# Kernel tuning notes

Measured on AMD Instinct MI355X. Metric: run time of the kernel, lower is better.

The kernel has to match this reference:

```python
import jax, jax.numpy as jnp
import numpy as np

H_Q = 32      # num_attention_heads
H_KV = 8      # num_key_value_heads
D = 128       # head_dim
WIN = 127     # left window size (flash window_size=(127,-1))
BLK = 128


def setup_inputs() -> dict:
    key = jax.random.key(0)
    kq, kk, kv = jax.random.split(key, 3)
    B, S = 2, 4096
    Q = jax.random.normal(kq, (B, S, H_Q * D), dtype=jnp.float32)
    K = jax.random.normal(kk, (B, S, H_KV * D), dtype=jnp.float32)
    V = jax.random.normal(kv, (B, S, H_KV * D), dtype=jnp.float32)
    return {"Q": Q, "K": K, "V": V}


def _banded_mask(nblk):
    # query row r in block n has global index n*BLK + r
    # key col c in window indexes global key (n-1)*BLK + c,  c in [0, 2*BLK)
    r = jnp.arange(BLK)[:, None]
    c = jnp.arange(2 * BLK)[None, :]
    base = (c <= r + BLK) & (c >= r + BLK - WIN)          # [BLK, 2BLK]
    n = jnp.arange(nblk)[:, None, None]
    valid_pad = (n > 0) | (c[None] >= BLK)                # block 0 has zero-padded left keys
    return base[None] & valid_pad                          # [nblk, BLK, 2BLK]


def reference(Q, K, V):
    B, S, _ = Q.shape
    nblk = S // BLK
    g = H_Q // H_KV
    scale = 1.0 / np.sqrt(D)

    # [B, Hkv, g, nblk, BLK, D]
    q = Q.reshape(B, S, H_Q, D).transpose(0, 2, 1, 3).reshape(B, H_KV, g, nblk, BLK, D)
    k = K.reshape(B, S, H_KV, D).transpose(0, 2, 1, 3)   # [B, Hkv, S, D]
    v = V.reshape(B, S, H_KV, D).transpose(0, 2, 1, 3)

    # pad one zero block in front, then build 2-block sliding windows
    pad = jnp.zeros((B, H_KV, BLK, D), dtype=K.dtype)
    kp = jnp.concatenate([pad, k], axis=2).reshape(B, H_KV, nblk + 1, BLK, D)
    vp = jnp.concatenate([pad, v], axis=2).reshape(B, H_KV, nblk + 1, BLK, D)
    kwin = jnp.concatenate([kp[:, :, :-1], kp[:, :, 1:]], axis=3)  # [B,Hkv,nblk,2BLK,D]
    vwin = jnp.concatenate([vp[:, :, :-1], vp[:, :, 1:]], axis=3)

    scores = jnp.einsum('bhgnrd,bhncd->bhgnrc', q, kwin) * scale   # [B,Hkv,g,nblk,BLK,2BLK]
    mask = _banded_mask(nblk)                                      # [nblk,BLK,2BLK]
    scores = jnp.where(mask[None, None, None], scores, jnp.finfo(scores.dtype).min)
    p = jax.nn.softmax(scores, axis=-1)
    out = jnp.einsum('bhgnrc,bhncd->bhgnrd', p, vwin)              # [B,Hkv,g,nblk,BLK,D]
    out = out.reshape(B, H_Q, S, D).transpose(0, 2, 1, 3).reshape(B, S, H_Q * D)
    return out
```

## Files before the change

### kernel.cpp

```cpp
#include <hip/hip_runtime.h>
#include <stdint.h>

#define S_LEN 4096
#define HQ 32
#define HKV 8
#define DD 128
#define QBLK 128
#define KVROW (HKV * DD)

typedef __attribute__((ext_vector_type(8)))  __bf16 bf16x8;
typedef __attribute__((ext_vector_type(2)))  __bf16 bf16x2;
typedef __attribute__((ext_vector_type(4)))  float  f32x4;
typedef __attribute__((ext_vector_type(2)))  unsigned int u32x2;
typedef __attribute__((ext_vector_type(4)))  unsigned int u32x4;

__device__ __forceinline__ unsigned int pk2(float lo, float hi2) {
  bf16x2 t = {(__bf16)lo, (__bf16)hi2};
  return __builtin_bit_cast(unsigned int, t);
}
__device__ __forceinline__ bf16x8 mk8(unsigned int w0, unsigned int w1,
                                      unsigned int w2, unsigned int w3) {
  u32x4 u = {w0, w1, w2, w3};
  return __builtin_bit_cast(bf16x8, u);
}

#define SWZV(d) ((((d) & 7) ^ (((d) >> 4) & 7)) << 3)

__global__ __launch_bounds__(512, 4)
void swa_fwd(const float* __restrict__ Qg, const float* __restrict__ Kg,
             const float* __restrict__ Vg, float* __restrict__ Og) {
  __shared__ __align__(16) unsigned char Kl[40960];
  __shared__ __align__(16) unsigned char Vl[40960];

  const int nwg  = gridDim.x;
  const int bid0 = blockIdx.x;
  const int bid  = (bid0 & 7) * (nwg >> 3) + (bid0 >> 3);

  const int j    = bid & 3;
  const int n    = (bid >> 2) & 31;
  const int hkv  = (bid >> 7) & 7;
  const int b    = bid >> 10;
  const int tid  = threadIdx.x;
  const int lane = tid & 63;
  const int wv   = tid >> 6;
  const int g    = lane >> 4;
  const int l15  = lane & 15;

  const int cc = wv & 1;
  const int h  = hkv * 4 + (wv >> 1);
  const int cg = 2 * j + cc;
  const int qrow = n * QBLK + 32 * j + cc * 16 + l15;

  const float* qp = Qg + (size_t)(b * S_LEN + qrow) * (HQ * DD) + h * DD + g * 8;
  bf16x8 qf[4];
  #pragma unroll
  for (int dc = 0; dc < 4; ++dc) {
    f32x4 a  = *(const f32x4*)(qp + dc * 32);
    f32x4 c4 = *(const f32x4*)(qp + dc * 32 + 4);
    qf[dc] = mk8(pk2(a[0], a[1]), pk2(a[2], a[3]),
                 pk2(c4[0], c4[1]), pk2(c4[2], c4[3]));
  }

  const int kbase = (n - 1) * QBLK + 32 * j;
  #pragma unroll
  for (int i = 0; i < 10; ++i) {
    const int e  = i * 512 + tid;
    const int c  = e >> 5;
    const int dc = e & 31;
    int tk = kbase + c;
    tk = tk > 0 ? tk : 0;
    const size_t base = (size_t)(b * S_LEN + tk) * KVROW + hkv * DD + dc * 4;
    const f32x4 xk = *(const f32x4*)(Kg + base);
    const f32x4 xv = *(const f32x4*)(Vg + base);
    u32x2 kw = { pk2(xk[0], xk[1]), pk2(xk[2], xk[3]) };
    *(u32x2*)(&Kl[c * 256 + ((dc * 8) ^ ((c & 15) << 4))]) = kw;
    #pragma unroll
    for (int j4 = 0; j4 < 4; ++j4) {
      const int d = dc * 4 + j4;
      *(unsigned short*)(&Vl[d * 320 + ((c * 2) ^ SWZV(d))]) =
          __builtin_bit_cast(unsigned short, (__bf16)xv[j4]);
    }
  }
  __syncthreads();

  const float SC = 0.08838834764831845f * 1.44269504088896340f;

  f32x4 o[8];
  #pragma unroll
  for (int dt = 0; dt < 8; ++dt) o[dt] = (f32x4){0.f, 0.f, 0.f, 0.f};
  float ls = 0.f;

  #pragma unroll
  for (int pp = 0; pp < 5; ++pp) {
    const int tt0 = 2 * pp, tt1 = 2 * pp + 1;
    if (n == 0 && cg + tt1 < 8) continue;

    unsigned int w0 = 0, w1 = 0, w2 = 0, w3 = 0;

    if (!(n == 0 && cg + tt0 < 8)) {
      const int c = (cc + tt0) * 16 + l15;
      f32x4 acc = {0.f, 0.f, 0.f, 0.f};
      __builtin_amdgcn_s_setprio(1);
      #pragma unroll
      for (int dc = 0; dc < 4; ++dc) {
        const bf16x8 kf = *(const bf16x8*)(
            &Kl[c * 256 + ((dc * 64 + g * 16) ^ ((c & 15) << 4))]);
        acc = __builtin_amdgcn_mfma_f32_16x16x32_bf16(kf, qf[dc], acc, 0, 0, 0);
      }
      __builtin_amdgcn_s_setprio(0);
      float p[4];
      #pragma unroll
      for (int r = 0; r < 4; ++r) {
        const int g4r = g * 4 + r;
        const float e = __builtin_amdgcn_exp2f(acc[r] * SC);
        bool valid = true;
        if (pp == 0) valid = (g4r > l15);
        if (pp == 4) valid = (g4r <= l15);
        p[r] = valid ? e : 0.f;
        ls += p[r];
      }
      w0 = pk2(p[0], p[1]);
      w1 = pk2(p[2], p[3]);
    }

    if (pp < 4 && !(n == 0 && cg + tt1 < 8)) {
      const int c = (cc + tt1) * 16 + l15;
      f32x4 acc = {0.f, 0.f, 0.f, 0.f};
      __builtin_amdgcn_s_setprio(1);
      #pragma unroll
      for (int dc = 0; dc < 4; ++dc) {
        const bf16x8 kf = *(const bf16x8*)(
            &Kl[c * 256 + ((dc * 64 + g * 16) ^ ((c & 15) << 4))]);
        acc = __builtin_amdgcn_mfma_f32_16x16x32_bf16(kf, qf[dc], acc, 0, 0, 0);
      }
      __builtin_amdgcn_s_setprio(0);
      float p0 = __builtin_amdgcn_exp2f(acc[0] * SC);
      float p1 = __builtin_amdgcn_exp2f(acc[1] * SC);
      float p2 = __builtin_amdgcn_exp2f(acc[2] * SC);
      float p3 = __builtin_amdgcn_exp2f(acc[3] * SC);
      ls += p0 + p1 + p2 + p3;
      w2 = pk2(p0, p1);
      w3 = pk2(p2, p3);
    }

    const bf16x8 pf = mk8(w0, w1, w2, w3);
    const int ck0 = ((cc + tt0) * 16 + g * 4) * 2;
    const int ck1 = (pp < 4) ? ((cc + tt1) * 16 + g * 4) * 2 : ck0;
    __builtin_amdgcn_s_setprio(1);
    #pragma unroll
    for (int dt = 0; dt < 8; ++dt) {
      const int d  = dt * 16 + l15;
      const int rb = d * 320;
      const int sz = SWZV(d);
      const u32x2 a0 = *(const u32x2*)(&Vl[rb + (ck0 ^ sz)]);
      const u32x2 a1 = *(const u32x2*)(&Vl[rb + (ck1 ^ sz)]);
      const bf16x8 vf = mk8(a0[0], a0[1], a1[0], a1[1]);
      o[dt] = __builtin_amdgcn_mfma_f32_16x16x32_bf16(vf, pf, o[dt], 0, 0, 0);
    }
    __builtin_amdgcn_s_setprio(0);
  }

  ls += __shfl_xor(ls, 16);
  ls += __shfl_xor(ls, 32);
  const float inv = 1.0f / ls;

  float* op = Og + (size_t)(b * S_LEN + qrow) * (HQ * DD) + h * DD + g * 4;
  #pragma unroll
  for (int dt = 0; dt < 8; ++dt) {
    f32x4 v = o[dt];
    v[0] *= inv; v[1] *= inv; v[2] *= inv; v[3] *= inv;
    *(f32x4*)(op + dt * 16) = v;
  }
}

extern "C" void kernel_launch(void* const* d_in, const int* in_sizes, int n_in,
                              void* d_out, int out_size, void* d_ws, size_t ws_size,
                              hipStream_t stream) {
  const float* Q = (const float*)d_in[0];
  const float* K = (const float*)d_in[1];
  const float* V = (const float*)d_in[2];
  float* O = (float*)d_out;
  const int B = in_sizes[0] / (S_LEN * HQ * DD);
  const int nblocks = B * HKV * (S_LEN / QBLK) * 4;
  swa_fwd<<<dim3(nblocks), dim3(512), 0, stream>>>(Q, K, V, O);
}
```

Measured before the change: 92.37 us.

## Process all four query sub-blocks per workgroup with a rolling K/V ring buffer

Each workgroup now handles the whole 128-row query block in a loop of four 32-row steps instead of launching one workgroup per step. The 160-key K/V window lives in LDS as a ring: after each step, 32 new key rows are written over the oldest slot, and their global loads are issued before the current compute so the latency is hidden. This removes the redundant re-loading and bf16 conversion of overlapping K/V windows across the four former workgroups. In exchange the grid is 4x smaller (512 workgroups), parallelism drops, and two barriers are added per step.

New measurement: 79.78 us, median of 2. 13.6% less time.

```diff
diff --git a/kernel.cpp b/kernel.cpp
--- a/kernel.cpp
+++ b/kernel.cpp
@@ -36,10 +36,9 @@
   const int bid0 = blockIdx.x;
   const int bid  = (bid0 & 7) * (nwg >> 3) + (bid0 >> 3);
 
-  const int j    = bid & 3;
-  const int n    = (bid >> 2) & 31;
-  const int hkv  = (bid >> 7) & 7;
-  const int b    = bid >> 10;
+  const int n    = bid & 31;
+  const int hkv  = (bid >> 5) & 7;
+  const int b    = bid >> 8;
   const int tid  = threadIdx.x;
   const int lane = tid & 63;
   const int wv   = tid >> 6;
@@ -48,32 +47,22 @@
 
   const int cc = wv & 1;
   const int h  = hkv * 4 + (wv >> 1);
-  const int cg = 2 * j + cc;
-  const int qrow = n * QBLK + 32 * j + cc * 16 + l15;
-
-  const float* qp = Qg + (size_t)(b * S_LEN + qrow) * (HQ * DD) + h * DD + g * 8;
-  bf16x8 qf[4];
-  #pragma unroll
-  for (int dc = 0; dc < 4; ++dc) {
-    f32x4 a  = *(const f32x4*)(qp + dc * 32);
-    f32x4 c4 = *(const f32x4*)(qp + dc * 32 + 4);
-    qf[dc] = mk8(pk2(a[0], a[1]), pk2(a[2], a[3]),
-                 pk2(c4[0], c4[1]), pk2(c4[2], c4[3]));
-  }
-
-  const int kbase = (n - 1) * QBLK + 32 * j;
+
+  const int c0 = tid >> 5;
+  const int dc = tid & 31;
+  const size_t kvoff = hkv * DD + dc * 4;
+  const int kbase0 = (n - 1) * QBLK;
+
   #pragma unroll
   for (int i = 0; i < 10; ++i) {
-    const int e  = i * 512 + tid;
-    const int c  = e >> 5;
-    const int dc = e & 31;
-    int tk = kbase + c;
+    const int c = c0 + i * 16;
+    int tk = kbase0 + c;
     tk = tk > 0 ? tk : 0;
-    const size_t base = (size_t)(b * S_LEN + tk) * KVROW + hkv * DD + dc * 4;
+    const size_t base = (size_t)(b * S_LEN + tk) * KVROW + kvoff;
     const f32x4 xk = *(const f32x4*)(Kg + base);
     const f32x4 xv = *(const f32x4*)(Vg + base);
     u32x2 kw = { pk2(xk[0], xk[1]), pk2(xk[2], xk[3]) };
-    *(u32x2*)(&Kl[c * 256 + ((dc * 8) ^ ((c & 15) << 4))]) = kw;
+    *(u32x2*)(&Kl[c * 256 + ((dc * 8) ^ (c0 << 4))]) = kw;
     #pragma unroll
     for (int j4 = 0; j4 < 4; ++j4) {
       const int d = dc * 4 + j4;
@@ -85,91 +74,148 @@
 
   const float SC = 0.08838834764831845f * 1.44269504088896340f;
 
-  f32x4 o[8];
-  #pragma unroll
-  for (int dt = 0; dt < 8; ++dt) o[dt] = (f32x4){0.f, 0.f, 0.f, 0.f};
-  float ls = 0.f;
-
-  #pragma unroll
-  for (int pp = 0; pp < 5; ++pp) {
-    const int tt0 = 2 * pp, tt1 = 2 * pp + 1;
-    if (n == 0 && cg + tt1 < 8) continue;
-
-    unsigned int w0 = 0, w1 = 0, w2 = 0, w3 = 0;
-
-    if (!(n == 0 && cg + tt0 < 8)) {
-      const int c = (cc + tt0) * 16 + l15;
-      f32x4 acc = {0.f, 0.f, 0.f, 0.f};
-      __builtin_amdgcn_s_setprio(1);
+  #pragma unroll 1
+  for (int j = 0; j < 4; ++j) {
+    const int qrow = n * QBLK + 32 * j + cc * 16 + l15;
+    const float* qp = Qg + (size_t)(b * S_LEN + qrow) * (HQ * DD) + h * DD + g * 8;
+    f32x4 qa[4], qb[4];
+    #pragma unroll
+    for (int d4 = 0; d4 < 4; ++d4) {
+      qa[d4] = *(const f32x4*)(qp + d4 * 32);
+      qb[d4] = *(const f32x4*)(qp + d4 * 32 + 4);
+    }
+
+    f32x4 ik[2], iv[2];
+    if (j < 3) {
       #pragma unroll
-      for (int dc = 0; dc < 4; ++dc) {
-        const bf16x8 kf = *(const bf16x8*)(
-            &Kl[c * 256 + ((dc * 64 + g * 16) ^ ((c & 15) << 4))]);
-        acc = __builtin_amdgcn_mfma_f32_16x16x32_bf16(kf, qf[dc], acc, 0, 0, 0);
+      for (int ii = 0; ii < 2; ++ii) {
+        const int tk = kbase0 + 160 + 32 * j + c0 + 16 * ii;
+        const size_t base = (size_t)(b * S_LEN + tk) * KVROW + kvoff;
+        ik[ii] = *(const f32x4*)(Kg + base);
+        iv[ii] = *(const f32x4*)(Vg + base);
       }
-      __builtin_amdgcn_s_setprio(0);
-      float p[4];
+    }
+
+    bf16x8 qf[4];
+    #pragma unroll
+    for (int d4 = 0; d4 < 4; ++d4)
+      qf[d4] = mk8(pk2(qa[d4][0], qa[d4][1]), pk2(qa[d4][2], qa[d4][3]),
+                   pk2(qb[d4][0], qb[d4][1]), pk2(qb[d4][2], qb[d4][3]));
+
+    f32x4 o[8];
+    #pragma unroll
+    for (int dt = 0; dt < 8; ++dt) o[dt] = (f32x4){0.f, 0.f, 0.f, 0.f};
+    float ls = 0.f;
+
+    const int bt = 2 * j + cc;
+
+#define PAIR_BODY(pp)                                                         \
+    {                                                                         \
+      const int tt0 = 2 * (pp), tt1 = 2 * (pp) + 1;                           \
+      if (!(n == 0 && bt + tt1 < 8)) {                                        \
+        unsigned int w0 = 0, w1 = 0, w2 = 0, w3 = 0;                          \
+        int rt0 = bt + tt0; rt0 = (rt0 >= 10) ? rt0 - 10 : rt0;               \
+        int rt1 = bt + tt1; rt1 = (rt1 >= 10) ? rt1 - 10 : rt1;               \
+        if (!(n == 0 && bt + tt0 < 8)) {                                      \
+          const int c = rt0 * 16 + l15;                                       \
+          f32x4 acc = {0.f, 0.f, 0.f, 0.f};                                   \
+          __builtin_amdgcn_s_setprio(1);                                      \
+          _Pragma("unroll")                                                   \
+          for (int dcc = 0; dcc < 4; ++dcc) {                                 \
+            const bf16x8 kf = *(const bf16x8*)(                               \
+                &Kl[c * 256 + ((dcc * 64 + g * 16) ^ (l15 << 4))]);           \
+            acc = __builtin_amdgcn_mfma_f32_16x16x32_bf16(kf, qf[dcc], acc,   \
+                                                          0, 0, 0);           \
+          }                                                                   \
+          __builtin_amdgcn_s_setprio(0);                                      \
+          float p[4];                                                         \
+          _Pragma("unroll")                                                   \
+          for (int r = 0; r < 4; ++r) {                                       \
+            const int g4r = g * 4 + r;                                        \
+            const float e = __builtin_amdgcn_exp2f(acc[r] * SC);              \
+            bool valid = true;                                                \
+            if ((pp) == 0) valid = (g4r > l15);                               \
+            if ((pp) == 4) valid = (g4r <= l15);                              \
+            p[r] = valid ? e : 0.f;                                           \
+            ls += p[r];                                                       \
+          }                                                                   \
+          w0 = pk2(p[0], p[1]);                                               \
+          w1 = pk2(p[2], p[3]);                                               \
+        }                                                                     \
+        if ((pp) < 4 && !(n == 0 && bt + tt1 < 8)) {                          \
+          const int c = rt1 * 16 + l15;                                       \
+          f32x4 acc = {0.f, 0.f, 0.f, 0.f};                                   \
+          __builtin_amdgcn_s_setprio(1);                                      \
+          _Pragma("unroll")                                                   \
+          for (int dcc = 0; dcc < 4; ++dcc) {                                 \
+            const bf16x8 kf = *(const bf16x8*)(                               \
+                &Kl[c * 256 + ((dcc * 64 + g * 16) ^ (l15 << 4))]);           \
+            acc = __builtin_amdgcn_mfma_f32_16x16x32_bf16(kf, qf[dcc], acc,   \
+                                                          0, 0, 0);           \
+          }                                                                   \
+          __builtin_amdgcn_s_setprio(0);                                      \
+          float p0 = __builtin_amdgcn_exp2f(acc[0] * SC);                     \
+          float p1 = __builtin_amdgcn_exp2f(acc[1] * SC);                     \
+          float p2 = __builtin_amdgcn_exp2f(acc[2] * SC);                     \
+          float p3 = __builtin_amdgcn_exp2f(acc[3] * SC);                     \
+          ls += p0 + p1 + p2 + p3;                                            \
+          w2 = pk2(p0, p1);                                                   \
+          w3 = pk2(p2, p3);                                                   \
+        }                                                                     \
+        const bf16x8 pf = mk8(w0, w1, w2, w3);                                \
+        const int ck0 = (rt0 * 16 + g * 4) * 2;                               \
+        const int ck1 = ((pp) < 4) ? (rt1 * 16 + g * 4) * 2 : ck0;            \
+        __builtin_amdgcn_s_setprio(1);                                        \
+        _Pragma("unroll")                                                     \
+        for (int dt = 0; dt < 8; ++dt) {                                      \
+          const int d  = dt * 16 + l15;                                       \
+          const int rb = d * 320;                                             \
+          const int sz = SWZV(d);                                             \
+          const u32x2 a0 = *(const u32x2*)(&Vl[rb + (ck0 ^ sz)]);             \
+          const u32x2 a1 = *(const u32x2*)(&Vl[rb + (ck1 ^ sz)]);             \
+          const bf16x8 vf = mk8(a0[0], a0[1], a1[0], a1[1]);                  \
+          o[dt] = __builtin_amdgcn_mfma_f32_16x16x32_bf16(vf, pf, o[dt],      \
+                                                          0, 0, 0);           \
+        }                                                                     \
+        __builtin_amdgcn_s_setprio(0);                                        \
+      }                                                                       \
+    }
+
+    PAIR_BODY(0)
+    PAIR_BODY(1)
+    PAIR_BODY(2)
+    PAIR_BODY(3)
+    PAIR_BODY(4)
+#undef PAIR_BODY
+
+    ls += __shfl_xor(ls, 16);
+    ls += __shfl_xor(ls, 32);
+    const float inv = 1.0f / ls;
+
+    float* op = Og + (size_t)(b * S_LEN + qrow) * (HQ * DD) + h * DD + g * 4;
+    #pragma unroll
+    for (int dt = 0; dt < 8; ++dt) {
+      f32x4 v = o[dt];
+      v[0] *= inv; v[1] *= inv; v[2] *= inv; v[3] *= inv;
+      *(f32x4*)(op + dt * 16) = v;
+    }
+
+    if (j < 3) {
+      __syncthreads();
       #pragma unroll
-      for (int r = 0; r < 4; ++r) {
-        const int g4r = g * 4 + r;
-        const float e = __builtin_amdgcn_exp2f(acc[r] * SC);
-        bool valid = true;
-        if (pp == 0) valid = (g4r > l15);
-        if (pp == 4) valid = (g4r <= l15);
-        p[r] = valid ? e : 0.f;
-        ls += p[r];
+      for (int ii = 0; ii < 2; ++ii) {
+        const int r = 32 * j + c0 + 16 * ii;
+        u32x2 kw = { pk2(ik[ii][0], ik[ii][1]), pk2(ik[ii][2], ik[ii][3]) };
+        *(u32x2*)(&Kl[r * 256 + ((dc * 8) ^ (c0 << 4))]) = kw;
+        #pragma unroll
+        for (int j4 = 0; j4 < 4; ++j4) {
+          const int d = dc * 4 + j4;
+          *(unsigned short*)(&Vl[d * 320 + ((r * 2) ^ SWZV(d))]) =
+              __builtin_bit_cast(unsigned short, (__bf16)iv[ii][j4]);
+        }
       }
-      w0 = pk2(p[0], p[1]);
-      w1 = pk2(p[2], p[3]);
-    }
-
-    if (pp < 4 && !(n == 0 && cg + tt1 < 8)) {
-      const int c = (cc + tt1) * 16 + l15;
-      f32x4 acc = {0.f, 0.f, 0.f, 0.f};
-      __builtin_amdgcn_s_setprio(1);
-      #pragma unroll
-      for (int dc = 0; dc < 4; ++dc) {
-        const bf16x8 kf = *(const bf16x8*)(
-            &Kl[c * 256 + ((dc * 64 + g * 16) ^ ((c & 15) << 4))]);
-        acc = __builtin_amdgcn_mfma_f32_16x16x32_bf16(kf, qf[dc], acc, 0, 0, 0);
-      }
-      __builtin_amdgcn_s_setprio(0);
-      float p0 = __builtin_amdgcn_exp2f(acc[0] * SC);
-      float p1 = __builtin_amdgcn_exp2f(acc[1] * SC);
-      float p2 = __builtin_amdgcn_exp2f(acc[2] * SC);
-      float p3 = __builtin_amdgcn_exp2f(acc[3] * SC);
-      ls += p0 + p1 + p2 + p3;
-      w2 = pk2(p0, p1);
-      w3 = pk2(p2, p3);
-    }
-
-    const bf16x8 pf = mk8(w0, w1, w2, w3);
-    const int ck0 = ((cc + tt0) * 16 + g * 4) * 2;
-    const int ck1 = (pp < 4) ? ((cc + tt1) * 16 + g * 4) * 2 : ck0;
-    __builtin_amdgcn_s_setprio(1);
-    #pragma unroll
-    for (int dt = 0; dt < 8; ++dt) {
-      const int d  = dt * 16 + l15;
-      const int rb = d * 320;
-      const int sz = SWZV(d);
-      const u32x2 a0 = *(const u32x2*)(&Vl[rb + (ck0 ^ sz)]);
-      const u32x2 a1 = *(const u32x2*)(&Vl[rb + (ck1 ^ sz)]);
-      const bf16x8 vf = mk8(a0[0], a0[1], a1[0], a1[1]);
-      o[dt] = __builtin_amdgcn_mfma_f32_16x16x32_bf16(vf, pf, o[dt], 0, 0, 0);
-    }
-    __builtin_amdgcn_s_setprio(0);
-  }
-
-  ls += __shfl_xor(ls, 16);
-  ls += __shfl_xor(ls, 32);
-  const float inv = 1.0f / ls;
-
-  float* op = Og + (size_t)(b * S_LEN + qrow) * (HQ * DD) + h * DD + g * 4;
-  #pragma unroll
-  for (int dt = 0; dt < 8; ++dt) {
-    f32x4 v = o[dt];
-    v[0] *= inv; v[1] *= inv; v[2] *= inv; v[3] *= inv;
-    *(f32x4*)(op + dt * 16) = v;
+      __syncthreads();
+    }
   }
 }
 
@@ -181,6 +227,6 @@
   const float* V = (const float*)d_in[2];
   float* O = (float*)d_out;
   const int B = in_sizes[0] / (S_LEN * HQ * DD);
-  const int nblocks = B * HKV * (S_LEN / QBLK) * 4;
+  const int nblocks = B * HKV * (S_LEN / QBLK);
   swa_fwd<<<dim3(nblocks), dim3(512), 0, stream>>>(Q, K, V, O);
 }
```
